# Performance work log

Hardware: AMD Instinct MI355X
Metric: run time of the kernel (lower is better)

## Reference

```python
import jax, jax.numpy as jnp
import numpy as np

L, D, H, F, V, B, S = 2, 1024, 16, 4096, 32000, 1, 1024
EPS = 1e-6


def _layer_norm(x, scale, bias):
    mu = jnp.mean(x, axis=-1, keepdims=True)
    var = jnp.mean(jnp.square(x - mu), axis=-1, keepdims=True)
    return (x - mu) * jax.lax.rsqrt(var + EPS) * scale + bias


def _attention(x, mask, Wqkv, bqkv, Wo, bo):
    b, s, d = x.shape
    proj = x @ Wqkv + bqkv                      # [b, s, 3d]
    q, k, v = jnp.split(proj, 3, axis=-1)
    hd = d // H
    # NOTE: source uses a plain reshape (no transpose) to form heads -- replicate exactly.
    qh = q.reshape(b, H, s, hd)
    kh = k.reshape(b, H, s, hd)
    vh = v.reshape(b, H, s, hd)
    # NOTE: scale is 1/sqrt(hidden_dim), not 1/sqrt(head_dim), per source.
    scores = jnp.einsum('bhqd,bhkd->bhqk', qh, kh) / jnp.sqrt(jnp.asarray(d, x.dtype))
    scores = scores * mask                      # multiplicative mask, per source
    w = jax.nn.softmax(scores, axis=-1)
    ctx = jnp.einsum('bhqk,bhkd->bhqd', w, vh).reshape(b, s, d)
    return ctx @ Wo + bo, w


def _ffn(x, W1, b1, Wg, bg, W2, b2):
    h = x @ W1 + b1                             # [b, s, F]
    g = h @ Wg + bg                             # [b, s, 2F]
    a, gate = g[..., :F], g[..., F:]
    tanh_res = jnp.tanh(gate * 0.7978845608 * (1 + 0.044715 * gate ** 2))
    act = a * 0.5 * gate * (1 + tanh_res)
    return act @ W2 + b2


def setup_inputs() -> dict:
    key = jax.random.key(0)
    ks = jax.random.split(key, 16)

    def xav(k, shape):
        fan_in, fan_out = shape[-2], shape[-1]
        std = np.sqrt(2.0 / (fan_in + fan_out))
        return (jax.random.normal(k, shape, jnp.float32) * std)

    inp = {
        'tokens': jax.random.randint(ks[0], (B, S), 0, V, jnp.int32),
        'embed': jax.random.normal(ks[1], (V, D), jnp.float32) * 0.02,
        # per-layer params stacked on a leading L axis
        'qkv1_w': xav(ks[2], (L, D, 3 * D)), 'qkv1_b': jnp.zeros((L, 3 * D), jnp.float32),
        'out1_w': xav(ks[3], (L, D, D)),     'out1_b': jnp.zeros((L, D), jnp.float32),
        'qkv2_w': xav(ks[4], (L, D, 3 * D)), 'qkv2_b': jnp.zeros((L, 3 * D), jnp.float32),
        'out2_w': xav(ks[5], (L, D, D)),     'out2_b': jnp.zeros((L, D), jnp.float32),
        'ln1_s': jnp.ones((L, D), jnp.float32), 'ln1_b': jnp.zeros((L, D), jnp.float32),
        'ln2_s': jnp.ones((L, D), jnp.float32), 'ln2_b': jnp.zeros((L, D), jnp.float32),
        'ln3_s': jnp.ones((L, D), jnp.float32), 'ln3_b': jnp.zeros((L, D), jnp.float32),
        'ffn1_w': xav(ks[6], (L, D, F)),     'ffn1_b': jnp.zeros((L, F), jnp.float32),
        'ffng_w': xav(ks[7], (L, F, 2 * F)), 'ffng_b': jnp.zeros((L, 2 * F), jnp.float32),
        'ffn2_w': xav(ks[8], (L, F, D)),     'ffn2_b': jnp.zeros((L, D), jnp.float32),
        'head_w': xav(ks[9], (D, V)),        'head_b': jnp.zeros((V,), jnp.float32),
    }
    return inp


def reference(tokens, embed, qkv1_w, qkv1_b, out1_w, out1_b, qkv2_w, qkv2_b,
              out2_w, out2_b, ln1_s, ln1_b, ln2_s, ln2_b, ln3_s, ln3_b,
              ffn1_w, ffn1_b, ffng_w, ffng_b, ffn2_w, ffn2_b, head_w, head_b):
    x = embed[tokens]                                   # [B, S, D]
    idx = jnp.arange(S)
    mask = (idx[:, None] >= idx[None, :]).astype(x.dtype)[None, None]  # [1,1,S,S]

    att1_maps, att2_maps = [], []
    for l in range(L):
        x = _layer_norm(x, ln1_s[l], ln1_b[l])
        a1, w1 = _attention(x, mask, qkv1_w[l], qkv1_b[l], out1_w[l], out1_b[l])
        x = x + a1                                       # dropout is identity (eval)
        x = _layer_norm(x, ln2_s[l], ln2_b[l])
        a2, w2 = _attention(x, mask, qkv2_w[l], qkv2_b[l], out2_w[l], out2_b[l])
        x = x + a2
        xn = _layer_norm(x, ln3_s[l], ln3_b[l])
        ff = _ffn(xn, ffn1_w[l], ffn1_b[l], ffng_w[l], ffng_b[l], ffn2_w[l], ffn2_b[l])
        x = ff + a2                                      # residual from attention output, per source
        att1_maps.append(w1)
        att2_maps.append(w2)

    logits = x @ head_w + head_b                         # [B, S, V]
    return logits, jnp.stack(att1_maps), jnp.stack(att2_maps)
```

## Files before the change

kernel.cpp:

```cpp
#include <hip/hip_runtime.h>
#include <math.h>

#define S_ 1024
#define D_ 1024
#define H_ 16
#define F_ 4096
#define V_ 32000
#define L_ 2

typedef __attribute__((ext_vector_type(8))) short short8;
typedef __attribute__((ext_vector_type(4))) float f32x4;

__device__ __forceinline__ float wsum(float v) {
#pragma unroll
    for (int o = 32; o; o >>= 1) v += __shfl_xor(v, o);
    return v;
}
__device__ __forceinline__ float wmax(float v) {
#pragma unroll
    for (int o = 32; o; o >>= 1) v = fmaxf(v, __shfl_xor(v, o));
    return v;
}

__device__ __forceinline__ unsigned f2bf2(float lo, float hi) {
    unsigned a = __builtin_bit_cast(unsigned, lo);
    unsigned b = __builtin_bit_cast(unsigned, hi);
    a = (a + 0x7FFFu + ((a >> 16) & 1u)) >> 16;
    b = (b + 0x7FFFu + ((b >> 16) & 1u)) >> 16;
    return a | (b << 16);
}

__global__ __launch_bounds__(256) void k_embed(const int* __restrict__ tok,
                                               const float* __restrict__ emb,
                                               float* __restrict__ x) {
    int i = blockIdx.x * 256 + threadIdx.x;
    int row = i >> 8;
    int c4 = i & 255;
    ((float4*)x)[i] = ((const float4*)(emb + (long)tok[row] * D_))[c4];
}

__global__ __launch_bounds__(256) void k_ln(const float* __restrict__ x,
                                            const float* __restrict__ sc,
                                            const float* __restrict__ bi,
                                            float* __restrict__ y) {
    int row = blockIdx.x;
    int tid = threadIdx.x;
    float4 v = ((const float4*)(x + (long)row * D_))[tid];
    __shared__ float red[4];
    float s = v.x + v.y + v.z + v.w;
    s = wsum(s);
    if ((tid & 63) == 0) red[tid >> 6] = s;
    __syncthreads();
    float mu = (red[0] + red[1] + red[2] + red[3]) * (1.0f / D_);
    float dx = v.x - mu, dy = v.y - mu, dz = v.z - mu, dw = v.w - mu;
    float q = dx * dx + dy * dy + dz * dz + dw * dw;
    __syncthreads();
    q = wsum(q);
    if ((tid & 63) == 0) red[tid >> 6] = q;
    __syncthreads();
    float var = (red[0] + red[1] + red[2] + red[3]) * (1.0f / D_);
    float rstd = rsqrtf(var + 1e-6f);
    float4 sv = ((const float4*)sc)[tid];
    float4 bv = ((const float4*)bi)[tid];
    float4 o;
    o.x = dx * rstd * sv.x + bv.x;
    o.y = dy * rstd * sv.y + bv.y;
    o.z = dz * rstd * sv.z + bv.z;
    o.w = dw * rstd * sv.w + bv.w;
    ((float4*)(y + (long)row * D_))[tid] = o;
}

__global__ __launch_bounds__(256) void k_bgemm(const float* __restrict__ A, int lda,
                                               const float* __restrict__ B, int ldb,
                                               float* __restrict__ C, int ldc,
                                               const float* __restrict__ bias, int K) {
    __shared__ ushort Al[128][40];
    __shared__ ushort Bl[128][40];
    int tid = threadIdx.x;
    int lane = tid & 63;
    int wv = tid >> 6;
    int wr = wv >> 1, wc = wv & 1;
    int l15 = lane & 15, ko = (lane >> 4) << 3;
    int bm = blockIdx.y << 7, bn = blockIdx.x << 7;

    int arow = tid >> 1, akh = (tid & 1) << 4;
    int bn0 = (tid & 31) << 2, bkq = (tid >> 5) << 2;

    const float* Ap = A + (long)(bm + arow) * lda + akh;
    const float* Bp = B + (long)bkq * ldb + bn + bn0;

    f32x4 acc[4][4];
#pragma unroll
    for (int i = 0; i < 4; i++)
#pragma unroll
        for (int j = 0; j < 4; j++) acc[i][j] = (f32x4)0.0f;

    for (int k0 = 0; k0 < K; k0 += 32) {
        float4 a0 = *(const float4*)(Ap + k0);
        float4 a1 = *(const float4*)(Ap + k0 + 4);
        float4 a2 = *(const float4*)(Ap + k0 + 8);
        float4 a3 = *(const float4*)(Ap + k0 + 12);
        const float* bp = Bp + (long)k0 * ldb;
        float4 b0 = *(const float4*)(bp);
        float4 b1 = *(const float4*)(bp + ldb);
        float4 b2 = *(const float4*)(bp + 2 * (long)ldb);
        float4 b3 = *(const float4*)(bp + 3 * (long)ldb);
        __syncthreads();
        uint4 w0, w1;
        w0.x = f2bf2(a0.x, a0.y); w0.y = f2bf2(a0.z, a0.w);
        w0.z = f2bf2(a1.x, a1.y); w0.w = f2bf2(a1.z, a1.w);
        w1.x = f2bf2(a2.x, a2.y); w1.y = f2bf2(a2.z, a2.w);
        w1.z = f2bf2(a3.x, a3.y); w1.w = f2bf2(a3.z, a3.w);
        *(uint4*)&Al[arow][akh] = w0;
        *(uint4*)&Al[arow][akh + 8] = w1;
        uint2 t;
        t.x = f2bf2(b0.x, b1.x); t.y = f2bf2(b2.x, b3.x);
        *(uint2*)&Bl[bn0 + 0][bkq] = t;
        t.x = f2bf2(b0.y, b1.y); t.y = f2bf2(b2.y, b3.y);
        *(uint2*)&Bl[bn0 + 1][bkq] = t;
        t.x = f2bf2(b0.z, b1.z); t.y = f2bf2(b2.z, b3.z);
        *(uint2*)&Bl[bn0 + 2][bkq] = t;
        t.x = f2bf2(b0.w, b1.w); t.y = f2bf2(b2.w, b3.w);
        *(uint2*)&Bl[bn0 + 3][bkq] = t;
        __syncthreads();
        short8 af[4], bf[4];
#pragma unroll
        for (int m = 0; m < 4; m++)
            af[m] = *(short8*)&Al[(wr << 6) + (m << 4) + l15][ko];
#pragma unroll
        for (int n = 0; n < 4; n++)
            bf[n] = *(short8*)&Bl[(wc << 6) + (n << 4) + l15][ko];
#pragma unroll
        for (int m = 0; m < 4; m++)
#pragma unroll
            for (int n = 0; n < 4; n++)
                acc[m][n] = __builtin_amdgcn_mfma_f32_16x16x32_bf16(af[m], bf[n], acc[m][n], 0, 0, 0);
    }
    int r4 = (lane >> 4) << 2;
#pragma unroll
    for (int m = 0; m < 4; m++) {
#pragma unroll
        for (int n = 0; n < 4; n++) {
            int col = bn + (wc << 6) + (n << 4) + l15;
            float bv = bias ? bias[col] : 0.0f;
            int row = bm + (wr << 6) + (m << 4) + r4;
            float* cp = C + (long)row * ldc + col;
            cp[0] = acc[m][n][0] + bv;
            cp[(long)ldc] = acc[m][n][1] + bv;
            cp[2 * (long)ldc] = acc[m][n][2] + bv;
            cp[3 * (long)ldc] = acc[m][n][3] + bv;
        }
    }
}

__device__ __forceinline__ long hoff(int h, int sp, int colBase) {
    return (long)((h << 6) + (sp >> 4)) * (3 * D_) + colBase + ((sp & 15) << 6);
}

__global__ __launch_bounds__(256) void k_scores(const float* __restrict__ qkv,
                                                float* __restrict__ w) {
    int h = blockIdx.z;
    int bk = blockIdx.x << 6, bq = blockIdx.y << 6;
    __shared__ float Qs[64][65];
    __shared__ float Ks[64][65];
    int tid = threadIdx.x;
    int tx = tid & 15, ty = tid >> 4;
    int lrow = tid >> 2;
    int c0 = (tid & 3) << 4;
    {
        const float* qp = qkv + hoff(h, bq + lrow, 0);
        const float* kp = qkv + hoff(h, bk + lrow, D_);
#pragma unroll
        for (int u = 0; u < 4; u++) {
            float4 v = *(const float4*)(qp + c0 + u * 4);
            Qs[c0 + u * 4 + 0][lrow] = v.x;
            Qs[c0 + u * 4 + 1][lrow] = v.y;
            Qs[c0 + u * 4 + 2][lrow] = v.z;
            Qs[c0 + u * 4 + 3][lrow] = v.w;
            float4 kv = *(const float4*)(kp + c0 + u * 4);
            Ks[c0 + u * 4 + 0][lrow] = kv.x;
            Ks[c0 + u * 4 + 1][lrow] = kv.y;
            Ks[c0 + u * 4 + 2][lrow] = kv.z;
            Ks[c0 + u * 4 + 3][lrow] = kv.w;
        }
    }
    __syncthreads();
    int ty4 = ty << 2, tx4 = tx << 2;
    float acc[4][4] = {};
#pragma unroll 16
    for (int e = 0; e < 64; e++) {
        float q0 = Qs[e][ty4 + 0], q1 = Qs[e][ty4 + 1];
        float q2 = Qs[e][ty4 + 2], q3 = Qs[e][ty4 + 3];
        float k0 = Ks[e][tx4 + 0], k1 = Ks[e][tx4 + 1];
        float k2 = Ks[e][tx4 + 2], k3 = Ks[e][tx4 + 3];
        acc[0][0] += q0 * k0; acc[0][1] += q0 * k1; acc[0][2] += q0 * k2; acc[0][3] += q0 * k3;
        acc[1][0] += q1 * k0; acc[1][1] += q1 * k1; acc[1][2] += q1 * k2; acc[1][3] += q1 * k3;
        acc[2][0] += q2 * k0; acc[2][1] += q2 * k1; acc[2][2] += q2 * k2; acc[2][3] += q2 * k3;
        acc[3][0] += q3 * k0; acc[3][1] += q3 * k1; acc[3][2] += q3 * k2; acc[3][3] += q3 * k3;
    }
    const float scale = 0.03125f;
#pragma unroll
    for (int i = 0; i < 4; i++) {
        int qi = bq + ty4 + i;
        float4 o;
        o.x = (qi >= bk + tx4 + 0) ? acc[i][0] * scale : 0.0f;
        o.y = (qi >= bk + tx4 + 1) ? acc[i][1] * scale : 0.0f;
        o.z = (qi >= bk + tx4 + 2) ? acc[i][2] * scale : 0.0f;
        o.w = (qi >= bk + tx4 + 3) ? acc[i][3] * scale : 0.0f;
        *(float4*)(w + ((long)h * S_ + qi) * S_ + bk + tx4) = o;
    }
}

__global__ __launch_bounds__(256) void k_softmax(float* __restrict__ w) {
    long row = blockIdx.x;
    float* p = w + row * S_;
    int tid = threadIdx.x;
    float4 v = ((float4*)p)[tid];
    __shared__ float red[4];
    float m = fmaxf(fmaxf(v.x, v.y), fmaxf(v.z, v.w));
    m = wmax(m);
    if ((tid & 63) == 0) red[tid >> 6] = m;
    __syncthreads();
    m = fmaxf(fmaxf(red[0], red[1]), fmaxf(red[2], red[3]));
    v.x = expf(v.x - m); v.y = expf(v.y - m);
    v.z = expf(v.z - m); v.w = expf(v.w - m);
    float s = v.x + v.y + v.z + v.w;
    __syncthreads();
    s = wsum(s);
    if ((tid & 63) == 0) red[tid >> 6] = s;
    __syncthreads();
    float inv = 1.0f / (red[0] + red[1] + red[2] + red[3]);
    v.x *= inv; v.y *= inv; v.z *= inv; v.w *= inv;
    ((float4*)p)[tid] = v;
}

__global__ __launch_bounds__(256) void k_pv(const float* __restrict__ w,
                                            const float* __restrict__ qkv,
                                            float* __restrict__ ctx) {
    int h = blockIdx.y;
    int bm = blockIdx.x << 6;
    const float* A = w + (long)h * S_ * S_;
    __shared__ float As[16][65];
    __shared__ float Bs[16][64];
    int tid = threadIdx.x;
    int tx = tid & 15, ty = tid >> 4;
    int arow = tid >> 2, acol = (tid & 3) << 2;
    int brow = tid >> 4, bcol = (tid & 15) << 2;
    int ty4 = ty << 2, tx4 = tx << 2;
    float acc[4][4] = {};
    for (int k0 = 0; k0 < S_; k0 += 16) {
        float4 av = *(const float4*)(A + (long)(bm + arow) * S_ + k0 + acol);
        float4 bv = *(const float4*)(qkv + hoff(h, k0 + brow, 2 * D_) + bcol);
        __syncthreads();
        As[acol + 0][arow] = av.x;
        As[acol + 1][arow] = av.y;
        As[acol + 2][arow] = av.z;
        As[acol + 3][arow] = av.w;
        *(float4*)&Bs[brow][bcol] = bv;
        __syncthreads();
#pragma unroll
        for (int kk = 0; kk < 16; kk++) {
            float a0 = As[kk][ty4 + 0], a1 = As[kk][ty4 + 1];
            float a2 = As[kk][ty4 + 2], a3 = As[kk][ty4 + 3];
            float b0 = Bs[kk][tx4 + 0], b1 = Bs[kk][tx4 + 1];
            float b2 = Bs[kk][tx4 + 2], b3 = Bs[kk][tx4 + 3];
            acc[0][0] += a0 * b0; acc[0][1] += a0 * b1; acc[0][2] += a0 * b2; acc[0][3] += a0 * b3;
            acc[1][0] += a1 * b0; acc[1][1] += a1 * b1; acc[1][2] += a1 * b2; acc[1][3] += a1 * b3;
            acc[2][0] += a2 * b0; acc[2][1] += a2 * b1; acc[2][2] += a2 * b2; acc[2][3] += a2 * b3;
            acc[3][0] += a3 * b0; acc[3][1] += a3 * b1; acc[3][2] += a3 * b2; acc[3][3] += a3 * b3;
        }
    }
#pragma unroll
    for (int i = 0; i < 4; i++) {
        int sp = bm + ty4 + i;
        float* cp = ctx + (long)((h << 6) + (sp >> 4)) * D_ + ((sp & 15) << 6) + tx4;
        float4 o;
        o.x = acc[i][0]; o.y = acc[i][1]; o.z = acc[i][2]; o.w = acc[i][3];
        *(float4*)cp = o;
    }
}

__global__ __launch_bounds__(256) void k_add(float* __restrict__ dst,
                                             const float* __restrict__ a,
                                             const float* __restrict__ b) {
    int i = blockIdx.x * 256 + threadIdx.x;
    float4 x = ((const float4*)a)[i];
    float4 y = ((const float4*)b)[i];
    x.x += y.x; x.y += y.y; x.z += y.z; x.w += y.w;
    ((float4*)dst)[i] = x;
}

__device__ __forceinline__ float geglu1(float a, float g) {
    float t = tanhf(g * 0.7978845608f * (1.0f + 0.044715f * g * g));
    return a * 0.5f * g * (1.0f + t);
}
__global__ __launch_bounds__(256) void k_geglu(const float* __restrict__ g,
                                               float* __restrict__ act) {
    int i = blockIdx.x * 256 + threadIdx.x;
    int row = i >> 10;
    int c4 = i & 1023;
    const float* base = g + (long)row * (2 * F_);
    float4 a = ((const float4*)base)[c4];
    float4 gt = ((const float4*)(base + F_))[c4];
    float4 o;
    o.x = geglu1(a.x, gt.x);
    o.y = geglu1(a.y, gt.y);
    o.z = geglu1(a.z, gt.z);
    o.w = geglu1(a.w, gt.w);
    ((float4*)act)[i] = o;
}

extern "C" void kernel_launch(void* const* d_in, const int* in_sizes, int n_in,
                              void* d_out, int out_size, void* d_ws, size_t ws_size,
                              hipStream_t stream) {
    const int* tokens = (const int*)d_in[0];
    const float* embed = (const float*)d_in[1];
    const float* qkv1_w = (const float*)d_in[2];
    const float* qkv1_b = (const float*)d_in[3];
    const float* out1_w = (const float*)d_in[4];
    const float* out1_b = (const float*)d_in[5];
    const float* qkv2_w = (const float*)d_in[6];
    const float* qkv2_b = (const float*)d_in[7];
    const float* out2_w = (const float*)d_in[8];
    const float* out2_b = (const float*)d_in[9];
    const float* ln1_s = (const float*)d_in[10];
    const float* ln1_b = (const float*)d_in[11];
    const float* ln2_s = (const float*)d_in[12];
    const float* ln2_b = (const float*)d_in[13];
    const float* ln3_s = (const float*)d_in[14];
    const float* ln3_b = (const float*)d_in[15];
    const float* ffn1_w = (const float*)d_in[16];
    const float* ffn1_b = (const float*)d_in[17];
    const float* ffng_w = (const float*)d_in[18];
    const float* ffng_b = (const float*)d_in[19];
    const float* ffn2_w = (const float*)d_in[20];
    const float* ffn2_b = (const float*)d_in[21];
    const float* head_w = (const float*)d_in[22];
    const float* head_b = (const float*)d_in[23];

    float* out = (float*)d_out;
    float* logits = out;
    float* att1 = out + (long)S_ * V_;
    float* att2 = att1 + (long)L_ * H_ * S_ * S_;

    float* ws = (float*)d_ws;
    float* x = ws;
    float* xn = x + 1048576;
    float* qkv = xn + 1048576;
    float* ctx = qkv + 3145728;
    float* attn = ctx + 1048576;
    float *hbuf, *gbuf, *abuf;
    size_t need = (size_t)23068672 * sizeof(float);
    if (ws_size >= need) {
        hbuf = attn + 1048576;
        gbuf = hbuf + 4194304;
        abuf = gbuf + 8388608;
    } else {
        hbuf = logits;
        gbuf = hbuf + 4194304;
        abuf = gbuf + 8388608;
    }

    k_embed<<<1024, 256, 0, stream>>>(tokens, embed, x);

    for (int l = 0; l < L_; l++) {
        for (int a = 0; a < 2; a++) {
            const float* lns = (a == 0 ? ln1_s : ln2_s) + (long)l * D_;
            const float* lnb = (a == 0 ? ln1_b : ln2_b) + (long)l * D_;
            const float* Wq = (a == 0 ? qkv1_w : qkv2_w) + (long)l * D_ * 3 * D_;
            const float* bq = (a == 0 ? qkv1_b : qkv2_b) + (long)l * 3 * D_;
            const float* Wo = (a == 0 ? out1_w : out2_w) + (long)l * D_ * D_;
            const float* bo = (a == 0 ? out1_b : out2_b) + (long)l * D_;
            float* wmap = (a == 0 ? att1 : att2) + (long)l * H_ * S_ * S_;

            k_ln<<<S_, 256, 0, stream>>>(x, lns, lnb, xn);
            k_bgemm<<<dim3(24, 8), 256, 0, stream>>>(xn, D_, Wq, 3 * D_, qkv, 3 * D_, bq, D_);
            k_scores<<<dim3(16, 16, 16), 256, 0, stream>>>(qkv, wmap);
            k_softmax<<<H_ * S_, 256, 0, stream>>>(wmap);
            k_pv<<<dim3(16, 16), 256, 0, stream>>>(wmap, qkv, ctx);
            k_bgemm<<<dim3(8, 8), 256, 0, stream>>>(ctx, D_, Wo, D_, attn, D_, bo, D_);
            k_add<<<1024, 256, 0, stream>>>(x, xn, attn);
        }
        k_ln<<<S_, 256, 0, stream>>>(x, ln3_s + (long)l * D_, ln3_b + (long)l * D_, xn);
        k_bgemm<<<dim3(32, 8), 256, 0, stream>>>(xn, D_, ffn1_w + (long)l * D_ * F_, F_,
                                                 hbuf, F_, ffn1_b + (long)l * F_, D_);
        k_bgemm<<<dim3(64, 8), 256, 0, stream>>>(hbuf, F_, ffng_w + (long)l * F_ * 2 * F_, 2 * F_,
                                                 gbuf, 2 * F_, ffng_b + (long)l * 2 * F_, F_);
        k_geglu<<<4096, 256, 0, stream>>>(gbuf, abuf);
        k_bgemm<<<dim3(8, 8), 256, 0, stream>>>(abuf, F_, ffn2_w + (long)l * F_ * D_, D_,
                                                hbuf, D_, ffn2_b + (long)l * D_, F_);
        k_add<<<1024, 256, 0, stream>>>(x, hbuf, attn);
    }

    k_bgemm<<<dim3(250, 8), 256, 0, stream>>>(x, D_, head_w, V_, logits, V_, head_b, D_);
}
```

Baseline: 2.607 ms.

## Pre-convert weights and activations to bf16 and use bf16-input GEMM kernel

Adds kernels that convert and transpose fp32 weights to bf16 (K-contiguous) and has LN, PV and GEGLU write bf16 activation copies. A new templated GEMM then loads bf16 directly instead of converting fp32 inside the main loop, and uses 512-thread tiles for the large FFN-gate and head GEMMs. Weight conversion runs on every call, which adds its own memory traffic. The path needs a larger workspace and falls back to the old path otherwise. Dead empty loops were also inserted into the old GEMM.

```diff
diff --git a/kernel.cpp b/kernel.cpp
--- a/kernel.cpp
+++ b/kernel.cpp
@@ -10,6 +10,7 @@
 
 typedef __attribute__((ext_vector_type(8))) short short8;
 typedef __attribute__((ext_vector_type(4))) float f32x4;
+typedef __attribute__((ext_vector_type(4))) unsigned short us4;
 
 __device__ __forceinline__ float wsum(float v) {
 #pragma unroll
@@ -22,12 +23,12 @@
     return v;
 }
 
+__device__ __forceinline__ unsigned short f2bf(float x) {
+    unsigned u = __builtin_bit_cast(unsigned, x);
+    return (unsigned short)((u + 0x7FFFu + ((u >> 16) & 1u)) >> 16);
+}
 __device__ __forceinline__ unsigned f2bf2(float lo, float hi) {
-    unsigned a = __builtin_bit_cast(unsigned, lo);
-    unsigned b = __builtin_bit_cast(unsigned, hi);
-    a = (a + 0x7FFFu + ((a >> 16) & 1u)) >> 16;
-    b = (b + 0x7FFFu + ((b >> 16) & 1u)) >> 16;
-    return a | (b << 16);
+    return (unsigned)f2bf(lo) | ((unsigned)f2bf(hi) << 16);
 }
 
 __global__ __launch_bounds__(256) void k_embed(const int* __restrict__ tok,
@@ -39,10 +40,41 @@
     ((float4*)x)[i] = ((const float4*)(emb + (long)tok[row] * D_))[c4];
 }
 
+__global__ __launch_bounds__(256) void k_f2b(const float* __restrict__ a,
+                                             unsigned short* __restrict__ b) {
+    int i = blockIdx.x * 256 + threadIdx.x;
+    float4 v = ((const float4*)a)[i];
+    us4 o = {f2bf(v.x), f2bf(v.y), f2bf(v.z), f2bf(v.w)};
+    *(us4*)(b + (long)i * 4) = o;
+}
+
+__global__ __launch_bounds__(256) void k_cvtw(const float* __restrict__ src,
+                                              unsigned short* __restrict__ dst,
+                                              int Kd, int Nd) {
+    __shared__ unsigned short T[64][72];
+    int t = threadIdx.x;
+    int bn = blockIdx.x << 6, bk = blockIdx.y << 6;
+    int r = t >> 2, cq = (t & 3) << 4;
+    const float* p = src + (long)(bk + r) * Nd + bn + cq;
+#pragma unroll
+    for (int u = 0; u < 4; u++) {
+        float4 v = *(const float4*)(p + u * 4);
+        T[cq + u * 4 + 0][r] = f2bf(v.x);
+        T[cq + u * 4 + 1][r] = f2bf(v.y);
+        T[cq + u * 4 + 2][r] = f2bf(v.z);
+        T[cq + u * 4 + 3][r] = f2bf(v.w);
+    }
+    __syncthreads();
+    unsigned short* q = dst + (long)(bn + r) * Kd + bk + cq;
+    *(short8*)q = *(short8*)&T[r][cq];
+    *(short8*)(q + 8) = *(short8*)&T[r][cq + 8];
+}
+
 __global__ __launch_bounds__(256) void k_ln(const float* __restrict__ x,
                                             const float* __restrict__ sc,
                                             const float* __restrict__ bi,
-                                            float* __restrict__ y) {
+                                            float* __restrict__ y,
+                                            unsigned short* __restrict__ yb) {
     int row = blockIdx.x;
     int tid = threadIdx.x;
     float4 v = ((const float4*)(x + (long)row * D_))[tid];
@@ -68,33 +100,121 @@
     o.z = dz * rstd * sv.z + bv.z;
     o.w = dw * rstd * sv.w + bv.w;
     ((float4*)(y + (long)row * D_))[tid] = o;
+    if (yb) {
+        us4 ob = {f2bf(o.x), f2bf(o.y), f2bf(o.z), f2bf(o.w)};
+        *(us4*)(yb + (long)row * D_ + tid * 4) = ob;
+    }
+}
+
+template <int WGM, int WGN, bool BF16C>
+__global__ __launch_bounds__(WGM* WGN * 64) void k_bg(
+    const unsigned short* __restrict__ A, int lda,
+    const unsigned short* __restrict__ Bt, int ldb,
+    void* __restrict__ Cp, int ldc, const float* __restrict__ bias, int K) {
+    constexpr int TH = WGM * WGN * 64;
+    constexpr int ABYTES = WGM * 4096;
+    constexpr int CH = (WGM + WGN) * 4096 / (TH * 16);
+    __shared__ unsigned short Al[WGM * 64][40];
+    __shared__ unsigned short Bl[WGN * 64][40];
+    int tid = threadIdx.x;
+    int lane = tid & 63;
+    int wv = tid >> 6;
+    int wr = wv >> 1, wc = wv & 1;
+    int l15 = lane & 15, ko = (lane >> 4) << 3;
+    int bm = blockIdx.y * (WGM * 64), bn = blockIdx.x * (WGN * 64);
+
+    int srow[CH], skc[CH];
+    bool sa[CH];
+#pragma unroll
+    for (int c = 0; c < CH; c++) {
+        int byte = (c * TH + tid) * 16;
+        sa[c] = byte < ABYTES;
+        int b2 = sa[c] ? byte : byte - ABYTES;
+        srow[c] = b2 >> 6;
+        skc[c] = (b2 & 63) >> 1;
+    }
+
+    f32x4 acc[4][4];
+#pragma unroll
+    for (int i = 0; i < 4; i++)
+#pragma unroll
+        for (int j = 0; j < 4; j++) acc[i][j] = (f32x4)0.0f;
+
+    for (int k0 = 0; k0 < K; k0 += 32) {
+        short8 v[CH];
+#pragma unroll
+        for (int c = 0; c < CH; c++) {
+            const unsigned short* g =
+                sa[c] ? A + (long)(bm + srow[c]) * lda + k0 + skc[c]
+                      : Bt + (long)(bn + srow[c]) * ldb + k0 + skc[c];
+            v[c] = *(const short8*)g;
+        }
+        __syncthreads();
+#pragma unroll
+        for (int c = 0; c < CH; c++) {
+            unsigned short* d = sa[c] ? &Al[srow[c]][skc[c]] : &Bl[srow[c]][skc[c]];
+            *(short8*)d = v[c];
+        }
+        __syncthreads();
+        short8 af[4], bf[4];
+#pragma unroll
+        for (int m = 0; m < 4; m++) af[m] = *(short8*)&Al[(wr << 6) + (m << 4) + l15][ko];
+#pragma unroll
+        for (int n = 0; n < 4; n++) bf[n] = *(short8*)&Bl[(wc << 6) + (n << 4) + l15][ko];
+#pragma unroll
+        for (int m = 0; m < 4; m++)
+#pragma unroll
+            for (int n = 0; n < 4; n++)
+                acc[m][n] = __builtin_amdgcn_mfma_f32_16x16x32_bf16(af[m], bf[n], acc[m][n], 0, 0, 0);
+    }
+    int r4 = (lane >> 4) << 2;
+#pragma unroll
+    for (int m = 0; m < 4; m++) {
+#pragma unroll
+        for (int n = 0; n < 4; n++) {
+            int col = bn + (wc << 6) + (n << 4) + l15;
+            float bv = bias ? bias[col] : 0.0f;
+            int row0 = bm + (wr << 6) + (m << 4) + r4;
+#pragma unroll
+            for (int j = 0; j < 4; j++) {
+                float val = acc[m][n][j] + bv;
+                if (BF16C)
+                    ((unsigned short*)Cp)[(long)(row0 + j) * ldc + col] = f2bf(val);
+                else
+                    ((float*)Cp)[(long)(row0 + j) * ldc + col] = val;
+            }
+        }
+    }
 }
 
 __global__ __launch_bounds__(256) void k_bgemm(const float* __restrict__ A, int lda,
                                                const float* __restrict__ B, int ldb,
                                                float* __restrict__ C, int ldc,
                                                const float* __restrict__ bias, int K) {
-    __shared__ ushort Al[128][40];
-    __shared__ ushort Bl[128][40];
+    __shared__ unsigned short Al[128][40];
+    __shared__ unsigned short Bl[128][40];
     int tid = threadIdx.x;
     int lane = tid & 63;
     int wv = tid >> 6;
     int wr = wv >> 1, wc = wv & 1;
     int l15 = lane & 15, ko = (lane >> 4) << 3;
     int bm = blockIdx.y << 7, bn = blockIdx.x << 7;
-
     int arow = tid >> 1, akh = (tid & 1) << 4;
     int bn0 = (tid & 31) << 2, bkq = (tid >> 5) << 2;
-
     const float* Ap = A + (long)(bm + arow) * lda + akh;
     const float* Bp = B + (long)bkq * ldb + bn + bn0;
-
     f32x4 acc[4][4];
 #pragma unroll
     for (int i = 0; i < 4; i++)
 #pragma unroll
         for (int j = 0; j < 4; j++) acc[i][j] = (f32x4)0.0f;
-
+    for (int k0 = 0; k0 < 0 + 1; k0 += 32) {}
+    for (int k0 = 0; k0 < 1024 * 0 + 0; k0 += 32) {}
+    for (int k0 = 0; k0 < 0; k0 += 32) {}
+    for (int k0 = 0; k0 < 0 + 0 + 0 + 0 + 0 + 0 + 0 + 0 + 0 + 0 + 0; k0 += 32) {}
+    for (int k0 = 0; k0 < 0; k0 += 32) {}
+    for (int k0 = 0; k0 < 0; k0 += 32) {}
+    for (int k0 = 0; k0 <  0; k0 += 32) {}
     for (int k0 = 0; k0 < K; k0 += 32) {
         float4 a0 = *(const float4*)(Ap + k0);
         float4 a1 = *(const float4*)(Ap + k0 + 4);
@@ -125,11 +245,9 @@
         __syncthreads();
         short8 af[4], bf[4];
 #pragma unroll
-        for (int m = 0; m < 4; m++)
-            af[m] = *(short8*)&Al[(wr << 6) + (m << 4) + l15][ko];
-#pragma unroll
-        for (int n = 0; n < 4; n++)
-            bf[n] = *(short8*)&Bl[(wc << 6) + (n << 4) + l15][ko];
+        for (int m = 0; m < 4; m++) af[m] = *(short8*)&Al[(wr << 6) + (m << 4) + l15][ko];
+#pragma unroll
+        for (int n = 0; n < 4; n++) bf[n] = *(short8*)&Bl[(wc << 6) + (n << 4) + l15][ko];
 #pragma unroll
         for (int m = 0; m < 4; m++)
 #pragma unroll
@@ -236,7 +354,8 @@
 
 __global__ __launch_bounds__(256) void k_pv(const float* __restrict__ w,
                                             const float* __restrict__ qkv,
-                                            float* __restrict__ ctx) {
+                                            float* __restrict__ ctxf,
+                                            unsigned short* __restrict__ ctxb) {
     int h = blockIdx.y;
     int bm = blockIdx.x << 6;
     const float* A = w + (long)h * S_ * S_;
@@ -273,10 +392,16 @@
 #pragma unroll
     for (int i = 0; i < 4; i++) {
         int sp = bm + ty4 + i;
-        float* cp = ctx + (long)((h << 6) + (sp >> 4)) * D_ + ((sp & 15) << 6) + tx4;
-        float4 o;
-        o.x = acc[i][0]; o.y = acc[i][1]; o.z = acc[i][2]; o.w = acc[i][3];
-        *(float4*)cp = o;
+        long off = (long)((h << 6) + (sp >> 4)) * D_ + ((sp & 15) << 6) + tx4;
+        if (ctxf) {
+            float4 o;
+            o.x = acc[i][0]; o.y = acc[i][1]; o.z = acc[i][2]; o.w = acc[i][3];
+            *(float4*)(ctxf + off) = o;
+        }
+        if (ctxb) {
+            us4 o = {f2bf(acc[i][0]), f2bf(acc[i][1]), f2bf(acc[i][2]), f2bf(acc[i][3])};
+            *(us4*)(ctxb + off) = o;
+        }
     }
 }
 
@@ -295,7 +420,8 @@
     return a * 0.5f * g * (1.0f + t);
 }
 __global__ __launch_bounds__(256) void k_geglu(const float* __restrict__ g,
-                                               float* __restrict__ act) {
+                                               float* __restrict__ actf,
+                                               unsigned short* __restrict__ actb) {
     int i = blockIdx.x * 256 + threadIdx.x;
     int row = i >> 10;
     int c4 = i & 1023;
@@ -307,7 +433,11 @@
     o.y = geglu1(a.y, gt.y);
     o.z = geglu1(a.z, gt.z);
     o.w = geglu1(a.w, gt.w);
-    ((float4*)act)[i] = o;
+    if (actf) ((float4*)actf)[i] = o;
+    if (actb) {
+        us4 ob = {f2bf(o.x), f2bf(o.y), f2bf(o.z), f2bf(o.w)};
+        *(us4*)(actb + (long)i * 4) = ob;
+    }
 }
 
 extern "C" void kernel_launch(void* const* d_in, const int* in_sizes, int n_in,
@@ -343,26 +473,86 @@
     float* att1 = out + (long)S_ * V_;
     float* att2 = att1 + (long)L_ * H_ * S_ * S_;
 
-    float* ws = (float*)d_ws;
-    float* x = ws;
+    float* fp = (float*)d_ws;
+    float* x = fp;
     float* xn = x + 1048576;
     float* qkv = xn + 1048576;
-    float* ctx = qkv + 3145728;
-    float* attn = ctx + 1048576;
-    float *hbuf, *gbuf, *abuf;
+    float* attn = qkv + 3145728;
+    float* gbuf = attn + 1048576;
+    unsigned short* us0 = (unsigned short*)(gbuf + 8388608);
+    unsigned short* ctxb = us0;
+    unsigned short* hbufb = ctxb + 1048576;
+    unsigned short* abufb = hbufb + 4194304;
+    unsigned short* xnb = abufb + 4194304;
+    unsigned short* xb = xnb + 1048576;
+    unsigned short* qkvt = xb + 1048576;
+    unsigned short* outt = qkvt + 3145728;
+    unsigned short* ffn1t = outt + 1048576;
+    unsigned short* ffn2t = ffn1t + 4194304;
+    unsigned short* ffngt = ffn2t + 4194304;
+    unsigned short* headt = ffngt;
+    size_t need_main = ((char*)(ffngt + 33554432)) - (char*)d_ws;
+
+    if (ws_size >= need_main) {
+        k_embed<<<1024, 256, 0, stream>>>(tokens, embed, x);
+
+        for (int l = 0; l < L_; l++) {
+            for (int a = 0; a < 2; a++) {
+                const float* lns = (a == 0 ? ln1_s : ln2_s) + (long)l * D_;
+                const float* lnb = (a == 0 ? ln1_b : ln2_b) + (long)l * D_;
+                const float* Wq = (a == 0 ? qkv1_w : qkv2_w) + (long)l * D_ * 3 * D_;
+                const float* bq = (a == 0 ? qkv1_b : qkv2_b) + (long)l * 3 * D_;
+                const float* Wo = (a == 0 ? out1_w : out2_w) + (long)l * D_ * D_;
+                const float* bo = (a == 0 ? out1_b : out2_b) + (long)l * D_;
+                float* wmap = (a == 0 ? att1 : att2) + (long)l * H_ * S_ * S_;
+
+                k_cvtw<<<dim3(48, 16), 256, 0, stream>>>(Wq, qkvt, D_, 3 * D_);
+                k_cvtw<<<dim3(16, 16), 256, 0, stream>>>(Wo, outt, D_, D_);
+                k_ln<<<S_, 256, 0, stream>>>(x, lns, lnb, xn, xnb);
+                k_bg<2, 2, false><<<dim3(24, 8), 256, 0, stream>>>(xnb, D_, qkvt, D_, qkv, 3 * D_, bq, D_);
+                k_scores<<<dim3(16, 16, 16), 256, 0, stream>>>(qkv, wmap);
+                k_softmax<<<H_ * S_, 256, 0, stream>>>(wmap);
+                k_pv<<<dim3(16, 16), 256, 0, stream>>>(wmap, qkv, nullptr, ctxb);
+                k_bg<2, 2, false><<<dim3(8, 8), 256, 0, stream>>>(ctxb, D_, outt, D_, attn, D_, bo, D_);
+                k_add<<<1024, 256, 0, stream>>>(x, xn, attn);
+            }
+            k_cvtw<<<dim3(64, 16), 256, 0, stream>>>(ffn1_w + (long)l * D_ * F_, ffn1t, D_, F_);
+            k_cvtw<<<dim3(128, 64), 256, 0, stream>>>(ffng_w + (long)l * F_ * 2 * F_, ffngt, F_, 2 * F_);
+            k_cvtw<<<dim3(16, 64), 256, 0, stream>>>(ffn2_w + (long)l * F_ * D_, ffn2t, F_, D_);
+            k_ln<<<S_, 256, 0, stream>>>(x, ln3_s + (long)l * D_, ln3_b + (long)l * D_, xn, xnb);
+            k_bg<2, 2, true><<<dim3(32, 8), 256, 0, stream>>>(xnb, D_, ffn1t, D_,
+                                                              hbufb, F_, ffn1_b + (long)l * F_, D_);
+            k_bg<4, 2, false><<<dim3(64, 4), 512, 0, stream>>>(hbufb, F_, ffngt, F_,
+                                                               gbuf, 2 * F_, ffng_b + (long)l * 2 * F_, F_);
+            k_geglu<<<4096, 256, 0, stream>>>(gbuf, nullptr, abufb);
+            k_bg<2, 2, false><<<dim3(8, 8), 256, 0, stream>>>(abufb, F_, ffn2t, F_,
+                                                              xn, D_, ffn2_b + (long)l * D_, F_);
+            k_add<<<1024, 256, 0, stream>>>(x, xn, attn);
+        }
+        k_cvtw<<<dim3(500, 16), 256, 0, stream>>>(head_w, headt, D_, V_);
+        k_f2b<<<1024, 256, 0, stream>>>(x, xb);
+        k_bg<4, 2, false><<<dim3(250, 4), 512, 0, stream>>>(xb, D_, headt, D_, logits, V_, head_b, D_);
+        return;
+    }
+
+    float* ws = (float*)d_ws;
+    float* x2 = ws;
+    float* xn2 = x2 + 1048576;
+    float* qkv2p = xn2 + 1048576;
+    float* ctx2 = qkv2p + 3145728;
+    float* attn2 = ctx2 + 1048576;
+    float *hbuf, *gbuf2, *abuf;
     size_t need = (size_t)23068672 * sizeof(float);
     if (ws_size >= need) {
-        hbuf = attn + 1048576;
-        gbuf = hbuf + 4194304;
-        abuf = gbuf + 8388608;
+        hbuf = attn2 + 1048576;
+        gbuf2 = hbuf + 4194304;
+        abuf = gbuf2 + 8388608;
     } else {
         hbuf = logits;
-        gbuf = hbuf + 4194304;
-        abuf = gbuf + 8388608;
-    }
-
-    k_embed<<<1024, 256, 0, stream>>>(tokens, embed, x);
-
+        gbuf2 = hbuf + 4194304;
+        abuf = gbuf2 + 8388608;
+    }
+    k_embed<<<1024, 256, 0, stream>>>(tokens, embed, x2);
     for (int l = 0; l < L_; l++) {
         for (int a = 0; a < 2; a++) {
             const float* lns = (a == 0 ? ln1_s : ln2_s) + (long)l * D_;
@@ -372,25 +562,23 @@
             const float* Wo = (a == 0 ? out1_w : out2_w) + (long)l * D_ * D_;
             const float* bo = (a == 0 ? out1_b : out2_b) + (long)l * D_;
             float* wmap = (a == 0 ? att1 : att2) + (long)l * H_ * S_ * S_;
-
-            k_ln<<<S_, 256, 0, stream>>>(x, lns, lnb, xn);
-            k_bgemm<<<dim3(24, 8), 256, 0, stream>>>(xn, D_, Wq, 3 * D_, qkv, 3 * D_, bq, D_);
-            k_scores<<<dim3(16, 16, 16), 256, 0, stream>>>(qkv, wmap);
+            k_ln<<<S_, 256, 0, stream>>>(x2, lns, lnb, xn2, nullptr);
+            k_bgemm<<<dim3(24, 8), 256, 0, stream>>>(xn2, D_, Wq, 3 * D_, qkv2p, 3 * D_, bq, D_);
+            k_scores<<<dim3(16, 16, 16), 256, 0, stream>>>(qkv2p, wmap);
             k_softmax<<<H_ * S_, 256, 0, stream>>>(wmap);
-            k_pv<<<dim3(16, 16), 256, 0, stream>>>(wmap, qkv, ctx);
-            k_bgemm<<<dim3(8, 8), 256, 0, stream>>>(ctx, D_, Wo, D_, attn, D_, bo, D_);
-            k_add<<<1024, 256, 0, stream>>>(x, xn, attn);
-        }
-        k_ln<<<S_, 256, 0, stream>>>(x, ln3_s + (long)l * D_, ln3_b + (long)l * D_, xn);
-        k_bgemm<<<dim3(32, 8), 256, 0, stream>>>(xn, D_, ffn1_w + (long)l * D_ * F_, F_,
+            k_pv<<<dim3(16, 16), 256, 0, stream>>>(wmap, qkv2p, ctx2, nullptr);
+            k_bgemm<<<dim3(8, 8), 256, 0, stream>>>(ctx2, D_, Wo, D_, attn2, D_, bo, D_);
+            k_add<<<1024, 256, 0, stream>>>(x2, xn2, attn2);
+        }
+        k_ln<<<S_, 256, 0, stream>>>(x2, ln3_s + (long)l * D_, ln3_b + (long)l * D_, xn2, nullptr);
+        k_bgemm<<<dim3(32, 8), 256, 0, stream>>>(xn2, D_, ffn1_w + (long)l * D_ * F_, F_,
                                                  hbuf, F_, ffn1_b + (long)l * F_, D_);
         k_bgemm<<<dim3(64, 8), 256, 0, stream>>>(hbuf, F_, ffng_w + (long)l * F_ * 2 * F_, 2 * F_,
-                                                 gbuf, 2 * F_, ffng_b + (long)l * 2 * F_, F_);
-        k_geglu<<<4096, 256, 0, stream>>>(gbuf, abuf);
+                                                 gbuf2, 2 * F_, ffng_b + (long)l * 2 * F_, F_);
+        k_geglu<<<4096, 256, 0, stream>>>(gbuf2, abuf, nullptr);
         k_bgemm<<<dim3(8, 8), 256, 0, stream>>>(abuf, F_, ffn2_w + (long)l * F_ * D_, D_,
                                                 hbuf, D_, ffn2_b + (long)l * D_, F_);
-        k_add<<<1024, 256, 0, stream>>>(x, hbuf, attn);
-    }
-
-    k_bgemm<<<dim3(250, 8), 256, 0, stream>>>(x, D_, head_w, V_, logits, V_, head_b, D_);
-}
+        k_add<<<1024, 256, 0, stream>>>(x2, hbuf, attn2);
+    }
+    k_bgemm<<<dim3(250, 8), 256, 0, stream>>>(x2, D_, head_w, V_, logits, V_, head_b, D_);
+}
```

New measurement: 2.263 ms. 1.15x faster.
